# Kernel optimization log

Measured on AMD Instinct MI355X. Metric: run time of the kernel, lower is better.

The kernel has to match this reference:

```python
import jax, jax.numpy as jnp
import numpy as np

MIN_DEPTH, MAX_DEPTH = 0.1, 100.0
BN_EPS = 1e-5


def _conv(x, w, b, pad):
    y = jax.lax.conv_general_dilated(
        x, w, window_strides=(1, 1), padding=[(pad, pad), (pad, pad)],
        dimension_numbers=("NCHW", "OIHW", "NCHW"))
    return y + b[None, :, None, None]


def _bn(x, gamma, beta, mean, var):
    # eval-mode BatchNorm2d with running stats
    inv = jax.lax.rsqrt(var + BN_EPS)
    return (x - mean[None, :, None, None]) * (gamma * inv)[None, :, None, None] + beta[None, :, None, None]


def _object_depths(depth, bboxes):
    # depth: (B,1,H,W), bboxes: (B,N,4) int — per-box median (lower median, like torch)
    B, _, H, W = depth.shape
    xs = jnp.arange(W)
    ys = jnp.arange(H)

    def per_image(d2, boxes):  # d2: (H,W), boxes: (N,4)
        dflat = d2.reshape(-1)

        def one_box(box):
            x1 = jnp.maximum(box[0], 0)
            y1 = jnp.maximum(box[1], 0)
            x2 = jnp.minimum(box[2], W)
            y2 = jnp.minimum(box[3], H)
            mask = (((ys >= y1) & (ys < y2))[:, None] & ((xs >= x1) & (xs < x2))[None, :]).reshape(-1)
            vals = jnp.where(mask, dflat, jnp.inf)
            s = jnp.sort(vals)
            k = mask.sum()
            idx = jnp.maximum((k - 1) // 2, 0)
            med = jnp.take(s, idx)
            return jnp.where(k > 0, med, jnp.zeros((), dtype=d2.dtype))

        return jax.vmap(one_box)(boxes)

    return jax.vmap(per_image)(depth[:, 0], bboxes)


def _forward(features, bboxes, w1, b1, g1, be1, m1, v1, w2, b2, g2, be2, m2, v2,
             w3, b3, uw1, ub1, uw2, ub2):
    # depth head
    h = jax.nn.relu(_bn(_conv(features, w1, b1, 1), g1, be1, m1, v1))
    h = jax.nn.relu(_bn(_conv(h, w2, b2, 1), g2, be2, m2, v2))
    disp = jax.nn.sigmoid(_conv(h, w3, b3, 0))  # (B,1,H,W)
    min_disp = 1.0 / MAX_DEPTH
    max_disp = 1.0 / MIN_DEPTH
    depth = 1.0 / (min_disp + (max_disp - min_disp) * disp)
    # uncertainty head
    u = jax.nn.relu(_conv(features, uw1, ub1, 1))
    uncertainty = jax.nn.softplus(_conv(u, uw2, ub2, 0))
    obj = _object_depths(depth, bboxes)
    return depth, uncertainty, obj


def setup_inputs() -> dict:
    key = jax.random.key(0)
    ks = jax.random.split(key, 16)
    B, C, Hc, H, W, N = 8, 256, 256, 96, 160, 64
    f32 = jnp.float32
    inp = {
        "features": jax.random.normal(ks[0], (B, C, H, W), dtype=f32),
        "bboxes": jax.random.randint(ks[1], (B, N, 4), 0, 96, dtype=jnp.int32),
        "w1": jax.random.normal(ks[2], (Hc, C, 3, 3), dtype=f32) * 0.02,
        "b1": jnp.zeros((Hc,), f32),
        "g1": jnp.ones((Hc,), f32),
        "be1": jnp.zeros((Hc,), f32),
        "m1": jax.random.normal(ks[3], (Hc,), dtype=f32) * 0.1,
        "v1": jnp.ones((Hc,), f32),
        "w2": jax.random.normal(ks[4], (Hc, Hc, 3, 3), dtype=f32) * 0.02,
        "b2": jnp.zeros((Hc,), f32),
        "g2": jnp.ones((Hc,), f32),
        "be2": jnp.zeros((Hc,), f32),
        "m2": jax.random.normal(ks[5], (Hc,), dtype=f32) * 0.1,
        "v2": jnp.ones((Hc,), f32),
        "w3": jax.random.normal(ks[6], (1, Hc, 1, 1), dtype=f32) * 0.05,
        "b3": jnp.zeros((1,), f32),
        "uw1": jax.random.normal(ks[7], (Hc // 2, C, 3, 3), dtype=f32) * 0.02,
        "ub1": jnp.zeros((Hc // 2,), f32),
        "uw2": jax.random.normal(ks[8], (1, Hc // 2, 1, 1), dtype=f32) * 0.05,
        "ub2": jnp.zeros((1,), f32),
    }
    return inp


def reference(features, bboxes, w1, b1, g1, be1, m1, v1, w2, b2, g2, be2, m2, v2,
              w3, b3, uw1, ub1, uw2, ub2):
    return _forward(features, bboxes, w1, b1, g1, be1, m1, v1, w2, b2, g2, be2,
                    m2, v2, w3, b3, uw1, ub1, uw2, ub2)
```

## Files before the change

### kernel.cpp

```cpp
#include <hip/hip_runtime.h>
#include <hip/hip_bf16.h>

#define HH 96
#define WW 160
#define BATCH 8
#define NPIX (BATCH*HH*WW)
#define CIN 256
#define IMG (HH*WW)
#define PW 162
#define PH 98
#define PR (PH*PW)
#define PTOT (BATCH*PR)

typedef short bf16x8 __attribute__((ext_vector_type(8)));
typedef float f32x4 __attribute__((ext_vector_type(4)));

__device__ __forceinline__ unsigned short f2bf(float f) {
    unsigned int u = __float_as_uint(f);
    u = (u + 0x7fffu + ((u >> 16) & 1u)) >> 16;
    return (unsigned short)u;
}

__device__ __forceinline__ void gload16(const void* g, void* l) {
    __builtin_amdgcn_global_load_lds(
        (const __attribute__((address_space(1))) void*)g,
        (__attribute__((address_space(3))) void*)l,
        16, 0, 0);
}

__global__ __launch_bounds__(256) void prep_scalars(
    const float* __restrict__ b1, const float* __restrict__ g1, const float* __restrict__ be1,
    const float* __restrict__ m1, const float* __restrict__ v1,
    const float* __restrict__ b2, const float* __restrict__ g2, const float* __restrict__ be2,
    const float* __restrict__ m2, const float* __restrict__ v2,
    const float* __restrict__ ub1,
    float* __restrict__ scale1, float* __restrict__ bias1,
    float* __restrict__ scale2, float* __restrict__ bias2)
{
    int t = threadIdx.x;
    float s1 = g1[t] * rsqrtf(v1[t] + 1e-5f);
    scale1[t] = s1;
    bias1[t]  = (b1[t] - m1[t]) * s1 + be1[t];
    float s2 = g2[t] * rsqrtf(v2[t] + 1e-5f);
    scale2[t] = s2;
    bias2[t]  = (b2[t] - m2[t]) * s2 + be2[t];
    if (t < 128) { scale1[256 + t] = 1.0f; bias1[256 + t] = ub1[t]; }
}

__global__ __launch_bounds__(256) void prep_weights(
    const float* __restrict__ w1, const float* __restrict__ w2, const float* __restrict__ uw1,
    unsigned short* __restrict__ w1T, unsigned short* __restrict__ w2T, unsigned short* __restrict__ uw1T)
{
    const int S = 256 * 2304;
    int i = blockIdx.x * 256 + threadIdx.x;
    if (i < S) {
        int co = i / 2304, r = i % 2304, pos = r >> 8, ci = r & 255;
        w1T[i] = f2bf(w1[(co * 256 + ci) * 9 + pos]);
    } else if (i < 2 * S) {
        int j = i - S;
        int co = j / 2304, r = j % 2304, pos = r >> 8, ci = r & 255;
        w2T[j] = f2bf(w2[(co * 256 + ci) * 9 + pos]);
    } else {
        int j = i - 2 * S;
        int co = j / 2304, r = j % 2304, pos = r >> 8, ci = r & 255;
        uw1T[j] = f2bf(uw1[(co * 256 + ci) * 9 + pos]);
    }
}

__global__ __launch_bounds__(128) void zero_pads(
    unsigned int* __restrict__ featP, unsigned int* __restrict__ h1P)
{
    int bid = blockIdx.x;
    unsigned int* buf = (bid < 4128) ? featP : h1P;
    int k = (bid < 4128) ? bid : (bid - 4128);
    int img = k / 516, i = k % 516;
    int py, px;
    if (i < PW)            { py = 0;      px = i; }
    else if (i < 2 * PW)   { py = PH - 1; px = i - PW; }
    else { int q = i - 2 * PW; py = 1 + (q >> 1); px = (q & 1) ? (PW - 1) : 0; }
    size_t row = (size_t)img * PR + (size_t)py * PW + px;
    buf[row * 128 + threadIdx.x] = 0;
}

__global__ __launch_bounds__(256) void pack_features(
    const float* __restrict__ f, unsigned short* __restrict__ ft)
{
    __shared__ float tile[32][33];
    int x0 = blockIdx.x * 32;
    int c0 = blockIdx.y * 32;
    int by = blockIdx.z;
    int b = by / HH, y = by % HH;
    int tx = threadIdx.x & 31, tg = threadIdx.x >> 5;
    const float* src = f + (((size_t)(b * CIN + c0) * HH + y) * WW) + x0;
    #pragma unroll
    for (int i = 0; i < 4; ++i) {
        int cl = tg + i * 8;
        tile[cl][tx] = src[(size_t)cl * HH * WW + tx];
    }
    __syncthreads();
    size_t rbase = (size_t)b * PR + (size_t)(y + 1) * PW + (x0 + 1);
    #pragma unroll
    for (int i = 0; i < 4; ++i) {
        int xl = tg + i * 8;
        ft[(rbase + xl) * 256 + c0 + tx] = f2bf(tile[tx][xl]);
    }
}

__global__ __launch_bounds__(256) void conv3x3_mfma(
    const unsigned short* __restrict__ inP,
    const unsigned short* __restrict__ wT,
    const float* __restrict__ scale, const float* __restrict__ bias,
    unsigned short* __restrict__ outT,
    float* __restrict__ uout,
    const float* __restrict__ uw2, const float* __restrict__ ub2,
    int Cout, int mode, int My)
{
    __shared__ unsigned short Alds[2][3 * 128 * 32];
    __shared__ unsigned short Blds[2][144 * 32];
    __shared__ float usum[2][128];

    const int t = threadIdx.x;
    const int wave = t >> 6;
    const int l = t & 63;

    const int lid = blockIdx.x;
    const int xcd = lid & 7;
    const int j = lid >> 3;
    const int n0 = (xcd * 120 + j / My) * 128;
    const int m0 = (j % My) * 128;
    const bool is_unc = (mode == 1) && (m0 == 256);

    const int b0 = n0 / IMG;
    const int rem0 = n0 % IMG;
    const int y0 = rem0 / WW;
    const int x0 = rem0 % WW;
    const int r0 = b0 * PR + (y0 + 1) * PW + (x0 + 1);

    const int lrow = l >> 2;
    const int lkq = (l & 3) ^ ((l >> 3) & 3);

    const unsigned short* asrc0 = wT + (size_t)(m0 + wave * 32 + lrow) * 9 * 256 + lkq * 8;
    const unsigned short* asrc1 = asrc0 + (size_t)16 * 9 * 256;

    char* AldsB = (char*)Alds;
    char* BldsB = (char*)Blds;

    const int wm = wave >> 1, wn = wave & 1;
    const int quad = l >> 4, lane16 = l & 15;
    const int aoff = lane16 * 64 + ((quad ^ ((lane16 >> 1) & 3)) << 4);

    int browbase[4];
    #pragma unroll
    for (int i = 0; i < 4; ++i) {
        int jj = wn * 64 + i * 16 + lane16;
        browbase[i] = jj + ((x0 + jj) >= WW ? 2 : 0) + 7;
    }

    f32x4 acc[4][4];
    #pragma unroll
    for (int mt = 0; mt < 4; ++mt)
        #pragma unroll
        for (int nt = 0; nt < 4; ++nt)
            acc[mt][nt] = (f32x4){0.f, 0.f, 0.f, 0.f};

    auto STAGE = [&](int ccoff, int dyi, int sel) {
        const unsigned short* a0 = asrc0 + (dyi * 3) * 256 + ccoff;
        const unsigned short* a1 = asrc1 + (dyi * 3) * 256 + ccoff;
        char* ad = AldsB + sel * 24576 + wave * 2048;
        #pragma unroll
        for (int dxp = 0; dxp < 3; ++dxp) {
            gload16(a0 + dxp * 256, ad + dxp * 8192);
            gload16(a1 + dxp * 256, ad + dxp * 8192 + 1024);
        }
        const ptrdiff_t rs = (ptrdiff_t)r0 + (ptrdiff_t)(dyi - 1) * PW - 8;
        const unsigned short* bs = inP + (rs + lrow) * 256 + ccoff + lkq * 8
                                       + (size_t)wave * 8192;
        char* bd = BldsB + sel * 9216;
        gload16(bs, bd + wave * 2048);
        gload16(bs + 4096, bd + wave * 2048 + 1024);
        if (wave == 3) gload16(bs + 8192, bd + 8192);
    };

    STAGE(0, 0, 0);

    int cur = 0;
    int ccoffN = 0, dyiN = 1;
    for (int it = 0; it < 24; ++it) {
        if (it < 23) {
            STAGE(ccoffN, dyiN, cur ^ 1);
            if (++dyiN == 3) { dyiN = 0; ccoffN += 32; }
            if (wave == 3) { asm volatile("s_waitcnt vmcnt(9)" ::: "memory"); }
            else           { asm volatile("s_waitcnt vmcnt(8)" ::: "memory"); }
        } else {
            asm volatile("s_waitcnt vmcnt(0)" ::: "memory");
        }
        __builtin_amdgcn_s_barrier();
        asm volatile("" ::: "memory");

        __builtin_amdgcn_s_setprio(1);
        const char* Ab = AldsB + cur * 24576;
        const char* Bb = BldsB + cur * 9216;
        #pragma unroll
        for (int dx = 0; dx < 3; ++dx) {
            bf16x8 af[4], bfr[4];
            #pragma unroll
            for (int mt = 0; mt < 4; ++mt)
                af[mt] = *(const bf16x8*)(Ab + dx * 8192 + ((wm * 4 + mt) << 10) + aoff);
            #pragma unroll
            for (int i = 0; i < 4; ++i) {
                int row = browbase[i] + dx;
                int ba = (row << 6) + ((quad ^ ((row >> 1) & 3)) << 4);
                bfr[i] = *(const bf16x8*)(Bb + ba);
            }
            #pragma unroll
            for (int mt = 0; mt < 4; ++mt)
                #pragma unroll
                for (int nt = 0; nt < 4; ++nt)
                    acc[mt][nt] = __builtin_amdgcn_mfma_f32_16x16x32_bf16(
                        af[mt], bfr[nt], acc[mt][nt], 0, 0, 0);
        }
        __builtin_amdgcn_s_setprio(0);

        asm volatile("" ::: "memory");
        __builtin_amdgcn_s_barrier();
        cur ^= 1;
    }

    if (is_unc) {
        const float* ub = bias + 256;
        float s[4] = {0.f, 0.f, 0.f, 0.f};
        #pragma unroll
        for (int mt = 0; mt < 4; ++mt) {
            const int mg = wm * 64 + mt * 16 + quad * 4;
            const float4 bi = *(const float4*)&ub[mg];
            const float4 uw = *(const float4*)&uw2[mg];
            #pragma unroll
            for (int nt = 0; nt < 4; ++nt) {
                s[nt] += fmaxf(acc[mt][nt][0] + bi.x, 0.f) * uw.x
                       + fmaxf(acc[mt][nt][1] + bi.y, 0.f) * uw.y
                       + fmaxf(acc[mt][nt][2] + bi.z, 0.f) * uw.z
                       + fmaxf(acc[mt][nt][3] + bi.w, 0.f) * uw.w;
            }
        }
        #pragma unroll
        for (int nt = 0; nt < 4; ++nt) {
            s[nt] += __shfl_xor(s[nt], 16);
            s[nt] += __shfl_xor(s[nt], 32);
        }
        if (quad == 0) {
            #pragma unroll
            for (int nt = 0; nt < 4; ++nt)
                usum[wm][wn * 64 + nt * 16 + lane16] = s[nt];
        }
        __syncthreads();
        if (t < 128) {
            float x = usum[0][t] + usum[1][t] + ub2[0];
            uout[n0 + t] = fmaxf(x, 0.f) + log1pf(expf(-fabsf(x)));
        }
        return;
    }

    size_t obase[4];
    #pragma unroll
    for (int nt = 0; nt < 4; ++nt) {
        int n = n0 + wn * 64 + nt * 16 + lane16;
        if (mode == 1) {
            int b = n / IMG, rem = n % IMG, yy = rem / WW, xx = rem % WW;
            obase[nt] = ((size_t)(b * PH + yy + 1) * PW + (xx + 1)) * 256;
        } else {
            obase[nt] = (size_t)n * Cout;
        }
    }
    #pragma unroll
    for (int mt = 0; mt < 4; ++mt) {
        const int mg = m0 + wm * 64 + mt * 16 + quad * 4;
        const float4 sc = *(const float4*)&scale[mg];
        const float4 bi = *(const float4*)&bias[mg];
        #pragma unroll
        for (int nt = 0; nt < 4; ++nt) {
            ushort4 pk;
            pk.x = f2bf(fmaxf(acc[mt][nt][0] * sc.x + bi.x, 0.f));
            pk.y = f2bf(fmaxf(acc[mt][nt][1] * sc.y + bi.y, 0.f));
            pk.z = f2bf(fmaxf(acc[mt][nt][2] * sc.z + bi.z, 0.f));
            pk.w = f2bf(fmaxf(acc[mt][nt][3] * sc.w + bi.w, 0.f));
            *(ushort4*)&outT[obase[nt] + mg] = pk;
        }
    }
}

__global__ __launch_bounds__(256) void head_depth(
    const unsigned short* __restrict__ h2, const float* __restrict__ w3,
    const float* __restrict__ b3, float* __restrict__ out)
{
    __shared__ float ws[256];
    ws[threadIdx.x] = w3[threadIdx.x];
    __syncthreads();
    const int pix = blockIdx.x * 64 + (threadIdx.x >> 2);
    const int q = threadIdx.x & 3;
    const unsigned short* p = h2 + (size_t)pix * 256 + q * 64;
    float s = 0.f;
    #pragma unroll
    for (int i = 0; i < 64; i += 8) {
        uint4 v = *(const uint4*)(p + i);
        const float* wq = &ws[q * 64 + i];
        s += __uint_as_float(v.x << 16) * wq[0];
        s += __uint_as_float(v.x & 0xffff0000u) * wq[1];
        s += __uint_as_float(v.y << 16) * wq[2];
        s += __uint_as_float(v.y & 0xffff0000u) * wq[3];
        s += __uint_as_float(v.z << 16) * wq[4];
        s += __uint_as_float(v.z & 0xffff0000u) * wq[5];
        s += __uint_as_float(v.w << 16) * wq[6];
        s += __uint_as_float(v.w & 0xffff0000u) * wq[7];
    }
    s += __shfl_xor(s, 1);
    s += __shfl_xor(s, 2);
    if (q == 0) {
        float x = s + b3[0];
        float sig = 1.f / (1.f + expf(-x));
        out[pix] = 1.f / (0.01f + 9.99f * sig);
    }
}

__global__ __launch_bounds__(256) void median_kernel(
    const float* __restrict__ depth, const int* __restrict__ bboxes, float* __restrict__ obj)
{
    const int bi = blockIdx.x;
    const int b = bi >> 6;
    const int* bb = bboxes + (size_t)bi * 4;
    int x1 = max(bb[0], 0), y1 = max(bb[1], 0);
    int x2 = min(bb[2], WW), y2 = min(bb[3], HH);
    int w = x2 - x1, h = y2 - y1;
    if (w <= 0 || h <= 0) {
        if (threadIdx.x == 0) obj[bi] = 0.f;
        return;
    }
    const int wh = w * h;
    int tgt = (wh - 1) >> 1;
    const float* dbase = depth + (size_t)b * HH * WW;

    __shared__ unsigned int hist[256];
    __shared__ unsigned int sel_prefix, sel_target;
    unsigned int prefix = 0;

    for (int pass = 0; pass < 4; ++pass) {
        const int shift = 24 - 8 * pass;
        hist[threadIdx.x] = 0;
        __syncthreads();
        const unsigned int mask_high = (pass == 0) ? 0u : (0xFFFFFFFFu << (shift + 8));
        for (int idx = threadIdx.x; idx < wh; idx += 256) {
            int yy = y1 + idx / w, xx = x1 + idx % w;
            unsigned int uu = __float_as_uint(dbase[yy * WW + xx]);
            if ((uu & mask_high) == (prefix & mask_high))
                atomicAdd(&hist[(uu >> shift) & 255], 1u);
        }
        __syncthreads();
        if (threadIdx.x == 0) {
            unsigned int cum = 0;
            for (int bin = 0; bin < 256; ++bin) {
                unsigned int c = hist[bin];
                if (cum + c > (unsigned int)tgt) {
                    sel_target = (unsigned int)tgt - cum;
                    sel_prefix = prefix | ((unsigned int)bin << shift);
                    break;
                }
                cum += c;
            }
        }
        __syncthreads();
        prefix = sel_prefix;
        tgt = (int)sel_target;
    }
    if (threadIdx.x == 0) obj[bi] = __uint_as_float(prefix);
}

extern "C" void kernel_launch(void* const* d_in, const int* in_sizes, int n_in,
                              void* d_out, int out_size, void* d_ws, size_t ws_size,
                              hipStream_t stream) {
    const float* features = (const float*)d_in[0];
    const int*   bboxes   = (const int*)d_in[1];
    const float* w1  = (const float*)d_in[2];
    const float* b1  = (const float*)d_in[3];
    const float* g1  = (const float*)d_in[4];
    const float* be1 = (const float*)d_in[5];
    const float* m1  = (const float*)d_in[6];
    const float* v1  = (const float*)d_in[7];
    const float* w2  = (const float*)d_in[8];
    const float* b2  = (const float*)d_in[9];
    const float* g2  = (const float*)d_in[10];
    const float* be2 = (const float*)d_in[11];
    const float* m2  = (const float*)d_in[12];
    const float* v2  = (const float*)d_in[13];
    const float* w3  = (const float*)d_in[14];
    const float* b3  = (const float*)d_in[15];
    const float* uw1 = (const float*)d_in[16];
    const float* ub1 = (const float*)d_in[17];
    const float* uw2 = (const float*)d_in[18];
    const float* ub2 = (const float*)d_in[19];
    float* out = (float*)d_out;

    char* ws = (char*)d_ws;
    unsigned short* featP = (unsigned short*)(ws + 8192);
    unsigned short* h1P   = (unsigned short*)(ws + 65044480);
    unsigned short* h2    = (unsigned short*)(ws + 8192);
    unsigned short* w1T   = (unsigned short*)(ws + 130080768);
    unsigned short* uw1T  = w1T + 256 * 2304;
    unsigned short* w2T   = uw1T + 128 * 2304;
    float* scale1 = (float*)(w2T + 589824);
    float* bias1  = scale1 + 384;
    float* scale2 = bias1 + 384;
    float* bias2  = scale2 + 256;

    prep_scalars<<<1, 256, 0, stream>>>(b1, g1, be1, m1, v1, b2, g2, be2, m2, v2, ub1,
                                        scale1, bias1, scale2, bias2);
    prep_weights<<<5760, 256, 0, stream>>>(w1, w2, uw1, w1T, w2T, uw1T);
    zero_pads<<<8256, 128, 0, stream>>>((unsigned int*)featP, (unsigned int*)h1P);
    pack_features<<<dim3(WW / 32, CIN / 32, BATCH * HH), 256, 0, stream>>>(features, featP);

    conv3x3_mfma<<<2880, 256, 0, stream>>>(
        featP, w1T, scale1, bias1, h1P, out + NPIX, uw2, ub2, 256, 1, 3);
    conv3x3_mfma<<<1920, 256, 0, stream>>>(
        h1P, w2T, scale2, bias2, h2, nullptr, nullptr, nullptr, 256, 0, 2);

    head_depth<<<NPIX / 64, 256, 0, stream>>>(h2, w3, b3, out);
    median_kernel<<<BATCH * 64, 256, 0, stream>>>(out, bboxes, out + 2 * NPIX);
}
```

Baseline: 658.7 us.

## Load conv weights directly into registers and triple-buffer input tiles in LDS

Weight fragments are no longer staged through LDS. Each wave now loads its A operands straight from global memory into double-buffered registers, one iteration ahead. The B (input) tiles move to a triple-buffered LDS ring, which lets the trailing barrier of each iteration be dropped, and the K loop is fully unrolled. This cuts LDS traffic and one barrier per step, but adds many VGPRs for prefetched fragments and duplicates weight reads across waves. Launch bounds now request two blocks per CU, which risks spills.

```diff
diff --git a/kernel.cpp b/kernel.cpp
--- a/kernel.cpp
+++ b/kernel.cpp
@@ -106,7 +106,7 @@
     }
 }
 
-__global__ __launch_bounds__(256) void conv3x3_mfma(
+__global__ __launch_bounds__(256, 2) void conv3x3_mfma(
     const unsigned short* __restrict__ inP,
     const unsigned short* __restrict__ wT,
     const float* __restrict__ scale, const float* __restrict__ bias,
@@ -115,8 +115,7 @@
     const float* __restrict__ uw2, const float* __restrict__ ub2,
     int Cout, int mode, int My)
 {
-    __shared__ unsigned short Alds[2][3 * 128 * 32];
-    __shared__ unsigned short Blds[2][144 * 32];
+    __shared__ unsigned short Blds[3][144 * 32];
     __shared__ float usum[2][128];
 
     const int t = threadIdx.x;
@@ -139,15 +138,13 @@
     const int lrow = l >> 2;
     const int lkq = (l & 3) ^ ((l >> 3) & 3);
 
-    const unsigned short* asrc0 = wT + (size_t)(m0 + wave * 32 + lrow) * 9 * 256 + lkq * 8;
-    const unsigned short* asrc1 = asrc0 + (size_t)16 * 9 * 256;
-
-    char* AldsB = (char*)Alds;
-    char* BldsB = (char*)Blds;
-
     const int wm = wave >> 1, wn = wave & 1;
     const int quad = l >> 4, lane16 = l & 15;
-    const int aoff = lane16 * 64 + ((quad ^ ((lane16 >> 1) & 3)) << 4);
+
+    const char* aB = (const char*)wT +
+        ((size_t)(m0 + wm * 64 + lane16) * 2304 + (size_t)quad * 8) * 2;
+
+    char* BldsB = (char*)Blds;
 
     int browbase[4];
     #pragma unroll
@@ -163,15 +160,9 @@
         for (int nt = 0; nt < 4; ++nt)
             acc[mt][nt] = (f32x4){0.f, 0.f, 0.f, 0.f};
 
-    auto STAGE = [&](int ccoff, int dyi, int sel) {
-        const unsigned short* a0 = asrc0 + (dyi * 3) * 256 + ccoff;
-        const unsigned short* a1 = asrc1 + (dyi * 3) * 256 + ccoff;
-        char* ad = AldsB + sel * 24576 + wave * 2048;
-        #pragma unroll
-        for (int dxp = 0; dxp < 3; ++dxp) {
-            gload16(a0 + dxp * 256, ad + dxp * 8192);
-            gload16(a1 + dxp * 256, ad + dxp * 8192 + 1024);
-        }
+    bf16x8 afb[2][12];
+
+    auto STAGE_B = [&](int ccoff, int dyi, int sel) {
         const ptrdiff_t rs = (ptrdiff_t)r0 + (ptrdiff_t)(dyi - 1) * PW - 8;
         const unsigned short* bs = inP + (rs + lrow) * 256 + ccoff + lkq * 8
                                        + (size_t)wave * 8192;
@@ -181,16 +172,30 @@
         if (wave == 3) gload16(bs + 8192, bd + 8192);
     };
 
-    STAGE(0, 0, 0);
-
-    int cur = 0;
-    int ccoffN = 0, dyiN = 1;
+    STAGE_B(0, 0, 0);
+    #pragma unroll
+    for (int f = 0; f < 12; ++f) {
+        const int dx = f / 4, mt = f % 4;
+        afb[0][f] = *(const bf16x8*)(aB + mt * 73728 + dx * 512);
+    }
+
+    #pragma unroll
     for (int it = 0; it < 24; ++it) {
+        const int cur = it % 3;
+        const int pcur = it & 1;
         if (it < 23) {
-            STAGE(ccoffN, dyiN, cur ^ 1);
-            if (++dyiN == 3) { dyiN = 0; ccoffN += 32; }
-            if (wave == 3) { asm volatile("s_waitcnt vmcnt(9)" ::: "memory"); }
-            else           { asm volatile("s_waitcnt vmcnt(8)" ::: "memory"); }
+            const int itn = it + 1;
+            const int ccn = itn / 3, dyin = itn % 3;
+            STAGE_B(ccn * 32, dyin, itn % 3);
+            #pragma unroll
+            for (int f = 0; f < 12; ++f) {
+                const int dx = f / 4, mt = f % 4;
+                afb[pcur ^ 1][f] = *(const bf16x8*)(aB + mt * 73728
+                                                    + (dyin * 3 + dx) * 512 + ccn * 64);
+            }
+            __builtin_amdgcn_sched_barrier(0);
+            if (wave == 3) { asm volatile("s_waitcnt vmcnt(15)" ::: "memory"); }
+            else           { asm volatile("s_waitcnt vmcnt(14)" ::: "memory"); }
         } else {
             asm volatile("s_waitcnt vmcnt(0)" ::: "memory");
         }
@@ -198,14 +203,10 @@
         asm volatile("" ::: "memory");
 
         __builtin_amdgcn_s_setprio(1);
-        const char* Ab = AldsB + cur * 24576;
         const char* Bb = BldsB + cur * 9216;
         #pragma unroll
         for (int dx = 0; dx < 3; ++dx) {
-            bf16x8 af[4], bfr[4];
-            #pragma unroll
-            for (int mt = 0; mt < 4; ++mt)
-                af[mt] = *(const bf16x8*)(Ab + dx * 8192 + ((wm * 4 + mt) << 10) + aoff);
+            bf16x8 bfr[4];
             #pragma unroll
             for (int i = 0; i < 4; ++i) {
                 int row = browbase[i] + dx;
@@ -217,13 +218,9 @@
                 #pragma unroll
                 for (int nt = 0; nt < 4; ++nt)
                     acc[mt][nt] = __builtin_amdgcn_mfma_f32_16x16x32_bf16(
-                        af[mt], bfr[nt], acc[mt][nt], 0, 0, 0);
+                        afb[pcur][dx * 4 + mt], bfr[nt], acc[mt][nt], 0, 0, 0);
         }
         __builtin_amdgcn_s_setprio(0);
-
-        asm volatile("" ::: "memory");
-        __builtin_amdgcn_s_barrier();
-        cur ^= 1;
     }
 
     if (is_unc) {
```

Measured after the change: 1.009 ms. +53.2%, slower.
